# Kernel tuning notes

Measured on AMD Instinct MI355X. Metric: run time of the kernel, lower is better.

The kernel has to match this reference:

```python
import jax, jax.numpy as jnp
import numpy as np

N_NODES = 50000
N_EDGES = 800000
HEADS = 8
CH = 64


def setup_inputs() -> dict:
    key = jax.random.key(0)
    ks = jax.random.split(key, 30)
    rn = lambda k, shape, s=0.1: (jax.random.normal(k, shape, jnp.float32) * s)
    inp = {
        'x': jax.random.normal(ks[0], (N_NODES, 3), jnp.float32),
        'edge_index': jax.random.randint(ks[1], (2, N_EDGES), 0, N_NODES, jnp.int32),
        'edge_attr': jax.random.normal(ks[2], (N_EDGES, 1), jnp.float32),
        'return_attention_weights': 1,
        # node / residual encoders
        'Wn': rn(ks[3], (3, 64)), 'bn': jnp.zeros((64,), jnp.float32),
        'Wr': rn(ks[4], (3, 512)), 'br': jnp.zeros((512,), jnp.float32),
        'W1': rn(ks[5], (64, 512)), 'as1': rn(ks[6], (HEADS, CH)), 'ad1': rn(ks[7], (HEADS, CH)), 'bc1': jnp.zeros((512,), jnp.float32),
        'W2': rn(ks[8], (512, 512)), 'as2': rn(ks[9], (HEADS, CH)), 'ad2': rn(ks[10], (HEADS, CH)), 'bc2': jnp.zeros((512,), jnp.float32),
        'W3': rn(ks[11], (512, 512)), 'as3': rn(ks[12], (HEADS, CH)), 'ad3': rn(ks[13], (HEADS, CH)), 'bc3': jnp.zeros((64,), jnp.float32),
        # node head
        'Wo': rn(ks[14], (64, 2)), 'bo': jnp.zeros((2,), jnp.float32),
        # edge classifier MLP 136 -> 256 -> 2
        'Wm1': rn(ks[15], (136, 256)), 'bm1': jnp.zeros((256,), jnp.float32),
        'Wm2': rn(ks[16], (256, 2)), 'bm2': jnp.zeros((2,), jnp.float32),
    }
    return inp


def _gat(h, src, dst, W, a_src, a_dst, b, concat):
    """PyG GATConv (shared lin, edge_dim=None, eval-mode dropout)."""
    n = h.shape[0]
    g = (h @ W).reshape(n, HEADS, CH)                      # [N,H,C]
    asrc = jnp.sum(g * a_src[None], -1)                    # [N,H]
    adst = jnp.sum(g * a_dst[None], -1)                    # [N,H]
    e = jax.nn.leaky_relu(asrc[src] + adst[dst], 0.2)      # [E',H]
    m = jax.ops.segment_max(e, dst, num_segments=n)        # softmax per destination
    ex = jnp.exp(e - m[dst])
    s = jax.ops.segment_sum(ex, dst, num_segments=n)
    alpha = ex / s[dst]                                    # [E',H]
    out = jax.ops.segment_sum(g[src] * alpha[..., None], dst, num_segments=n)  # [N,H,C]
    out = out.reshape(n, HEADS * CH) if concat else out.mean(axis=1)
    return out + b, alpha


def reference(x, edge_index, edge_attr, return_attention_weights,
              Wn, bn, Wr, br,
              W1, as1, ad1, bc1,
              W2, as2, ad2, bc2,
              W3, as3, ad3, bc3,
              Wo, bo, Wm1, bm1, Wm2, bm2):
    n = x.shape[0]
    e_len = edge_attr.shape[0]
    src0, dst0 = edge_index[0], edge_index[1]
    # GATConv adds self loops internally
    loop = jnp.arange(n, dtype=edge_index.dtype)
    src = jnp.concatenate([src0, loop])
    dst = jnp.concatenate([dst0, loop])

    h = x @ Wn + bn          # node_encoder (dropout is eval identity)
    res = x @ Wr + br        # self.linear residual
    # edge_encoder output is unused by GATConv (edge_dim=None) -> no-op

    o, _ = _gat(h, src, dst, W1, as1, ad1, bc1, concat=True)
    o = jax.nn.elu(o) + res
    o, _ = _gat(o, src, dst, W2, as2, ad2, bc2, concat=True)
    o = jax.nn.elu(o) + res
    o, alpha = _gat(o, src, dst, W3, as3, ad3, bc3, concat=False)
    node_embedding = jax.nn.elu(o)                          # [N,64]

    x_out = node_embedding @ Wo + bo                        # [N,2]
    edge_embedding = jnp.concatenate(
        [node_embedding[src0], alpha[:e_len], node_embedding[dst0]], axis=-1)  # [E,136]
    edge_out = jax.nn.relu(edge_embedding @ Wm1 + bm1) @ Wm2 + bm2             # [E,2]
    return x_out, edge_out
```

## Files before the change

kernel.cpp:

```cpp
#include <hip/hip_runtime.h>
#include <hip/hip_bf16.h>
#include <math.h>

#define N_NODES 50000
#define NPAD    50048
#define N_EDGES 800000
#define EPRIME  (N_EDGES + N_NODES)
#define HEADS 8
#define CH 64
#define FDIM 512

typedef unsigned short ushort_t;
typedef __attribute__((ext_vector_type(8))) short bf16x8_t;
typedef __attribute__((ext_vector_type(4))) float f32x4_t;

__device__ __forceinline__ float bf2f(unsigned short u) {
  union { unsigned int i; float f; } v; v.i = ((unsigned int)u) << 16; return v.f;
}
__device__ __forceinline__ unsigned short f2bf(float f) {
  union { float f; unsigned int i; } v; v.f = f;
  unsigned int x = v.i;
  return (unsigned short)((x + 0x7fffu + ((x >> 16) & 1u)) >> 16);
}
__device__ __forceinline__ float ldf(const void* p, size_t idx, int isf32) {
  return isf32 ? ((const float*)p)[idx] : bf2f(((const ushort_t*)p)[idx]);
}
__device__ __forceinline__ void stf(void* p, size_t idx, float v, int isf32) {
  if (isf32) ((float*)p)[idx] = v;
  else       ((ushort_t*)p)[idx] = f2bf(v);
}
__device__ __forceinline__ float leakyf(float v) { return v >= 0.f ? v : 0.2f * v; }
__device__ __forceinline__ float eluf(float v)   { return v > 0.f ? v : expm1f(v); }

__device__ __forceinline__ float dpp_sum64(float x) {
  x += __int_as_float(__builtin_amdgcn_update_dpp(0, __float_as_int(x), 0xB1, 0xf, 0xf, false));
  x += __int_as_float(__builtin_amdgcn_update_dpp(0, __float_as_int(x), 0x4E, 0xf, 0xf, false));
  x += __int_as_float(__builtin_amdgcn_update_dpp(0, __float_as_int(x), 0x141, 0xf, 0xf, false));
  x += __int_as_float(__builtin_amdgcn_update_dpp(0, __float_as_int(x), 0x140, 0xf, 0xf, false));
  x += __int_as_float(__builtin_amdgcn_update_dpp(0, __float_as_int(x), 0x142, 0xa, 0xf, false));
  x += __int_as_float(__builtin_amdgcn_update_dpp(0, __float_as_int(x), 0x143, 0xc, 0xf, false));
  return x;
}

typedef const __attribute__((address_space(1))) unsigned int* gas1_t;
typedef __attribute__((address_space(3))) unsigned int* las3_t;
__device__ __forceinline__ void gll16(const ushort_t* g, ushort_t* l) {
  __builtin_amdgcn_global_load_lds((gas1_t)g, (las3_t)l, 16, 0, 0);
}

__global__ void detect_dtype(const void* Wn, int* flag) {
  if (blockIdx.x == 0 && threadIdx.x == 0) {
    const ushort_t* u = (const ushort_t*)Wn;
    int extreme = 0;
    for (int i = 0; i < 384; ++i) {
      float v = fabsf(bf2f(u[i]));
      if (v != 0.f && (v > 16.f || v < 6.1e-5f)) extreme++;
    }
    *flag = (extreme >= 20) ? 1 : 0;
  }
}

__global__ void convert_wt(const void* __restrict__ src, ushort_t* __restrict__ dst,
                           int K, int N, int boff, const int* __restrict__ dflag) {
  int isf32 = *dflag;
  int tid = blockIdx.x * blockDim.x + threadIdx.x;
  if (tid >= N * K) return;
  int n = tid / K, k = tid % K;
  dst[tid] = f2bf(ldf(src, (size_t)(boff + k) * N + n, isf32));
}

__global__ void convert_att(const void* s1, const void* d1, const void* s2, const void* d2,
                            const void* s3, const void* d3, ushort_t* __restrict__ dst,
                            const int* __restrict__ dflag) {
  int isf32 = *dflag;
  int tid = blockIdx.x * blockDim.x + threadIdx.x;
  if (tid >= 6 * 512) return;
  int which = tid >> 9, idx = tid & 511;
  const void* p = which == 0 ? s1 : which == 1 ? d1 : which == 2 ? s2
                : which == 3 ? d2 : which == 4 ? s3 : d3;
  dst[tid] = f2bf(ldf(p, idx, isf32));
}

__global__ void init_deg(int* deg, int* fill) {
  int n = blockIdx.x * blockDim.x + threadIdx.x;
  if (n < N_NODES) { deg[n] = 1; fill[n] = 0; }
}

__global__ void count_edges(const int* __restrict__ ei, int* deg) {
  int e = blockIdx.x * blockDim.x + threadIdx.x;
  if (e < N_EDGES) atomicAdd(&deg[ei[N_EDGES + e]], 1);
}

__global__ __launch_bounds__(1024) void scan1024(const int* __restrict__ deg,
                                                 int* __restrict__ rowptr) {
  const int CHUNK = (N_NODES + 1023) / 1024;
  int t = threadIdx.x;
  int wave = t >> 6, lane = t & 63;
  int lo = t * CHUNK;
  int hi = lo + CHUNK; if (hi > N_NODES) hi = N_NODES;
  int s = 0;
  for (int i = lo; i < hi; ++i) s += deg[i];
  int inc = s;
  #pragma unroll
  for (int off = 1; off < 64; off <<= 1) {
    int u = __shfl_up(inc, off);
    if (lane >= off) inc += u;
  }
  __shared__ int wsum[16];
  if (lane == 63) wsum[wave] = inc;
  __syncthreads();
  int wbase = 0;
  for (int w = 0; w < wave; ++w) wbase += wsum[w];
  int run = wbase + inc - s;
  for (int i = lo; i < hi; ++i) { rowptr[i] = run; run += deg[i]; }
  if (t == 1023) rowptr[N_NODES] = run;
}

__global__ void fill_csr(const int* __restrict__ ei, const int* __restrict__ rowptr,
                         int* fill, int* __restrict__ csr_src) {
  int e = blockIdx.x * blockDim.x + threadIdx.x;
  if (e >= EPRIME) return;
  int s, d;
  if (e < N_EDGES) { s = ei[e]; d = ei[N_EDGES + e]; }
  else             { s = d = e - N_EDGES; }
  int pos = rowptr[d] + atomicAdd(&fill[d], 1);
  csr_src[pos] = s;
}

__global__ void encode_h(const void* __restrict__ x, const void* __restrict__ Wn,
                         const void* __restrict__ bn, ushort_t* __restrict__ h,
                         const int* __restrict__ dflag) {
  int isf32 = *dflag;
  int tid = blockIdx.x * blockDim.x + threadIdx.x;
  if (tid >= N_NODES * 64) return;
  int n = tid >> 6, j = tid & 63;
  float x0 = ldf(x, n * 3 + 0, isf32), x1 = ldf(x, n * 3 + 1, isf32), x2 = ldf(x, n * 3 + 2, isf32);
  float v = x0 * ldf(Wn, j, isf32) + x1 * ldf(Wn, 64 + j, isf32)
          + x2 * ldf(Wn, 128 + j, isf32) + ldf(bn, j, isf32);
  h[tid] = f2bf(v);
}

__global__ __launch_bounds__(256) void gemm_bt(
    const ushort_t* __restrict__ A, const ushort_t* __restrict__ BT,
    ushort_t* __restrict__ C, int K, int ldc,
    const ushort_t* __restrict__ att, float* __restrict__ asrc, float* __restrict__ adst)
{
  __shared__ __align__(16) ushort_t As[128][32];
  __shared__ __align__(16) ushort_t Bs[128][32];
  int tid = threadIdx.x;
  int wave = tid >> 6, lane = tid & 63;
  int wr = wave >> 1, wc = wave & 1;
  int row0 = blockIdx.x * 128, col0 = blockIdx.y * 128;
  int fm = lane & 15, fq = lane >> 4;

  f32x4_t acc[4][4];
  #pragma unroll
  for (int i = 0; i < 4; ++i)
    #pragma unroll
    for (int j = 0; j < 4; ++j) acc[i][j] = (f32x4_t){0.f, 0.f, 0.f, 0.f};

  int srow = wave * 32 + (lane >> 2);
  int skel = (lane & 3) * 8;
  const ushort_t* aG0 = A  + (size_t)(row0 + srow) * K + skel;
  const ushort_t* aG1 = A  + (size_t)(row0 + srow + 16) * K + skel;
  const ushort_t* bG0 = BT + (size_t)(col0 + srow) * K + skel;
  const ushort_t* bG1 = BT + (size_t)(col0 + srow + 16) * K + skel;
  ushort_t* aL0 = &As[wave * 32][0];
  ushort_t* aL1 = &As[wave * 32 + 16][0];
  ushort_t* bL0 = &Bs[wave * 32][0];
  ushort_t* bL1 = &Bs[wave * 32 + 16][0];

  for (int k0 = 0; k0 < K; k0 += 32) {
    gll16(aG0 + k0, aL0);
    gll16(aG1 + k0, aL1);
    gll16(bG0 + k0, bL0);
    gll16(bG1 + k0, bL1);
    __syncthreads();
    bf16x8_t af[4], bfr[4];
    #pragma unroll
    for (int i = 0; i < 4; ++i) af[i]  = *(const bf16x8_t*)&As[64 * wr + 16 * i + fm][fq * 8];
    #pragma unroll
    for (int j = 0; j < 4; ++j) bfr[j] = *(const bf16x8_t*)&Bs[64 * wc + 16 * j + fm][fq * 8];
    #pragma unroll
    for (int i = 0; i < 4; ++i)
      #pragma unroll
      for (int j = 0; j < 4; ++j)
        acc[i][j] = __builtin_amdgcn_mfma_f32_16x16x32_bf16(af[i], bfr[j], acc[i][j], 0, 0, 0);
    __syncthreads();
  }

  int do_att = (att != nullptr);
  int head = 2 * blockIdx.y + wc;
  float sa[4], sd[4];
  if (do_att) {
    #pragma unroll
    for (int j = 0; j < 4; ++j) {
      int ch = 16 * j + fm;
      sa[j] = bf2f(att[head * CH + ch]);
      sd[j] = bf2f(att[512 + head * CH + ch]);
    }
  }

  #pragma unroll
  for (int i = 0; i < 4; ++i) {
    int rowb = row0 + 64 * wr + 16 * i + fq * 4;
    #pragma unroll
    for (int r = 0; r < 4; ++r) {
      int row = rowb + r;
      float ss = 0.f, dd = 0.f;
      #pragma unroll
      for (int j = 0; j < 4; ++j) {
        ushort_t uv = f2bf(acc[i][j][r]);
        C[(size_t)row * ldc + col0 + 64 * wc + 16 * j + fm] = uv;
        if (do_att) {
          float cv = bf2f(uv);
          ss += cv * sa[j];
          dd += cv * sd[j];
        }
      }
      if (do_att) {
        #pragma unroll
        for (int off = 8; off > 0; off >>= 1) {
          ss += __shfl_down(ss, off);
          dd += __shfl_down(dd, off);
        }
        if (fm == 0 && row < N_NODES) {
          asrc[row * HEADS + head] = ss;
          adst[row * HEADS + head] = dd;
        }
      }
    }
  }
}

__global__ __launch_bounds__(256) void aggregate(
    const int* __restrict__ rowptr, const int* __restrict__ csr_src,
    const float* __restrict__ asrc, const float* __restrict__ adst,
    float* __restrict__ sumv,
    const ushort_t* __restrict__ g,
    const void* __restrict__ x, const void* __restrict__ Wr,
    const void* __restrict__ br, const void* __restrict__ bc,
    ushort_t* __restrict__ out, int mean_mode,
    const void* __restrict__ Wo, const void* __restrict__ bo,
    void* __restrict__ outh, const int* __restrict__ dflag)
{
  int isf32 = *dflag;
  __shared__ float sx[3];
  int n = blockIdx.x;
  int t = threadIdx.x;
  if (t < 3) sx[t] = ldf(x, n * 3 + t, isf32);
  __syncthreads();

  int start = rowptr[n], end = rowptr[n + 1];
  int c0 = t * 2;
  int h  = t >> 5;
  int i0 = n * HEADS + h;
  float ad = adst[i0];

  float l = 0.f, a0 = 0.f, a1 = 0.f;
  int i = start;
  for (; i + 8 <= end; i += 8) {
    int s[8];
    #pragma unroll
    for (int k = 0; k < 8; ++k) s[k] = csr_src[i + k];
    float e[8];
    unsigned int gv[8];
    #pragma unroll
    for (int k = 0; k < 8; ++k) {
      e[k]  = asrc[s[k] * HEADS + h] + ad;
      gv[k] = *(const unsigned int*)(g + (size_t)s[k] * FDIM + c0);
    }
    #pragma unroll
    for (int k = 0; k < 8; ++k) {
      float p = __expf(leakyf(e[k]));
      l  += p;
      a0 += p * bf2f((ushort_t)(gv[k] & 0xffffu));
      a1 += p * bf2f((ushort_t)(gv[k] >> 16));
    }
  }
  for (; i + 2 <= end; i += 2) {
    int s0 = csr_src[i], s1 = csr_src[i + 1];
    float e0 = asrc[s0 * HEADS + h] + ad;
    float e1 = asrc[s1 * HEADS + h] + ad;
    unsigned int g0 = *(const unsigned int*)(g + (size_t)s0 * FDIM + c0);
    unsigned int g1 = *(const unsigned int*)(g + (size_t)s1 * FDIM + c0);
    float p0 = __expf(leakyf(e0)), p1 = __expf(leakyf(e1));
    l  += p0 + p1;
    a0 += p0 * bf2f((ushort_t)(g0 & 0xffffu)) + p1 * bf2f((ushort_t)(g1 & 0xffffu));
    a1 += p0 * bf2f((ushort_t)(g0 >> 16))     + p1 * bf2f((ushort_t)(g1 >> 16));
  }
  if (i < end) {
    int s0 = csr_src[i];
    float p0 = __expf(leakyf(asrc[s0 * HEADS + h] + ad));
    unsigned int g0 = *(const unsigned int*)(g + (size_t)s0 * FDIM + c0);
    l  += p0;
    a0 += p0 * bf2f((ushort_t)(g0 & 0xffffu));
    a1 += p0 * bf2f((ushort_t)(g0 >> 16));
  }
  a0 /= l;
  a1 /= l;
  if ((t & 31) == 0) sumv[i0] = 1.f / l;

  if (!mean_mode) {
    float r0 = sx[0] * ldf(Wr, c0, isf32)         + sx[1] * ldf(Wr, 512 + c0, isf32)
             + sx[2] * ldf(Wr, 1024 + c0, isf32)  + ldf(br, c0, isf32);
    float r1 = sx[0] * ldf(Wr, c0 + 1, isf32)     + sx[1] * ldf(Wr, 512 + c0 + 1, isf32)
             + sx[2] * ldf(Wr, 1024 + c0 + 1, isf32) + ldf(br, c0 + 1, isf32);
    unsigned int o0 = f2bf(eluf(a0 + ldf(bc, c0, isf32)) + r0);
    unsigned int o1 = f2bf(eluf(a1 + ldf(bc, c0 + 1, isf32)) + r1);
    *(unsigned int*)(out + (size_t)n * FDIM + c0) = o0 | (o1 << 16);
  } else {
    __shared__ float red[512];
    red[c0] = a0; red[c0 + 1] = a1;
    __syncthreads();
    if (t < 64) {
      float tot = 0.f;
      #pragma unroll
      for (int hh = 0; hh < 8; ++hh) tot += red[t + 64 * hh];
      ushort_t uv = f2bf(eluf(tot * 0.125f + ldf(bc, t, isf32)));
      out[(size_t)n * CH + t] = uv;
      float nv = bf2f(uv);
      float p0 = nv * ldf(Wo, t * 2 + 0, isf32);
      float p1 = nv * ldf(Wo, t * 2 + 1, isf32);
      float vv = (t & 1) ? p1 : p0;
      float ww = (t & 1) ? p0 : p1;
      vv += __shfl_xor(ww, 1);
      #pragma unroll
      for (int off = 2; off < 64; off <<= 1) vv += __shfl_xor(vv, off);
      if (t < 2) stf(outh, (size_t)n * 2 + t, vv + ldf(bo, t, isf32), isf32);
    }
  }
}

#define EPW 32
__global__ __launch_bounds__(256) void edge_head6(
    const int* __restrict__ ei, const float* __restrict__ asrc, const float* __restrict__ adst,
    const float* __restrict__ rsumv,
    const ushort_t* __restrict__ pq, const void* __restrict__ Wm1,
    const void* __restrict__ bm1, const void* __restrict__ Wm2,
    const void* __restrict__ bm2, void* __restrict__ out,
    const int* __restrict__ dflag)
{
  int isf32 = *dflag;
  int lane = threadIdx.x & 63;
  int c0 = lane * 4;
  int h = lane & 7;
  float w1r[8][4], w2a[4], w2b[4], b1r[4];
  #pragma unroll
  for (int hh = 0; hh < 8; ++hh)
    #pragma unroll
    for (int j = 0; j < 4; ++j)
      w1r[hh][j] = ldf(Wm1, (64 + hh) * 256 + c0 + j, isf32);
  #pragma unroll
  for (int j = 0; j < 4; ++j) {
    w2a[j] = ldf(Wm2, (c0 + j) * 2 + 0, isf32);
    w2b[j] = ldf(Wm2, (c0 + j) * 2 + 1, isf32);
    b1r[j] = ldf(bm1, c0 + j, isf32);
  }
  float bo0 = ldf(bm2, 0, isf32), bo1 = ldf(bm2, 1, isf32);

  int wid = blockIdx.x * 4 + (threadIdx.x >> 6);
  int e0 = wid * EPW;
  for (int e = e0; e < e0 + EPW; e += 2) {
    int eu = __builtin_amdgcn_readfirstlane(e);
    int sA = ei[eu],     dA = ei[N_EDGES + eu];
    int sB = ei[eu + 1], dB = ei[N_EDGES + eu + 1];
    float vA = asrc[sA * HEADS + h] + adst[dA * HEADS + h];
    float vB = asrc[sB * HEADS + h] + adst[dB * HEADS + h];
    float rsA = rsumv[dA * HEADS + h], rsB = rsumv[dB * HEADS + h];
    ushort4 pvA = *(const ushort4*)(pq + (size_t)sA * FDIM + c0);
    ushort4 qvA = *(const ushort4*)(pq + (size_t)dA * FDIM + 256 + c0);
    ushort4 pvB = *(const ushort4*)(pq + (size_t)sB * FDIM + c0);
    ushort4 qvB = *(const ushort4*)(pq + (size_t)dB * FDIM + 256 + c0);
    float aA = __expf(leakyf(vA)) * rsA;
    float aB = __expf(leakyf(vB)) * rsB;
    float alA[8], alB[8];
    #pragma unroll
    for (int hh = 0; hh < 8; ++hh) {
      alA[hh] = __int_as_float(__builtin_amdgcn_readlane(__float_as_int(aA), hh));
      alB[hh] = __int_as_float(__builtin_amdgcn_readlane(__float_as_int(aB), hh));
    }

    float accA0 = 0.f, accA1 = 0.f, accB0 = 0.f, accB1 = 0.f;
    float pA[4] = { bf2f(pvA.x), bf2f(pvA.y), bf2f(pvA.z), bf2f(pvA.w) };
    float qA[4] = { bf2f(qvA.x), bf2f(qvA.y), bf2f(qvA.z), bf2f(qvA.w) };
    float pB[4] = { bf2f(pvB.x), bf2f(pvB.y), bf2f(pvB.z), bf2f(pvB.w) };
    float qB[4] = { bf2f(qvB.x), bf2f(qvB.y), bf2f(qvB.z), bf2f(qvB.w) };
    #pragma unroll
    for (int j = 0; j < 4; ++j) {
      float hvA = pA[j] + qA[j] + b1r[j];
      float hvB = pB[j] + qB[j] + b1r[j];
      #pragma unroll
      for (int hh = 0; hh < 8; ++hh) {
        hvA += alA[hh] * w1r[hh][j];
        hvB += alB[hh] * w1r[hh][j];
      }
      hvA = fmaxf(hvA, 0.f);
      hvB = fmaxf(hvB, 0.f);
      accA0 += hvA * w2a[j]; accA1 += hvA * w2b[j];
      accB0 += hvB * w2a[j]; accB1 += hvB * w2b[j];
    }
    accA0 = dpp_sum64(accA0);
    accA1 = dpp_sum64(accA1);
    accB0 = dpp_sum64(accB0);
    accB1 = dpp_sum64(accB1);
    if (lane == 63) {
      stf(out, 100000 + (size_t)e * 2 + 0, accA0 + bo0, isf32);
      stf(out, 100000 + (size_t)e * 2 + 1, accA1 + bo1, isf32);
      stf(out, 100000 + (size_t)e * 2 + 2, accB0 + bo0, isf32);
      stf(out, 100000 + (size_t)e * 2 + 3, accB1 + bo1, isf32);
    }
  }
}

extern "C" void kernel_launch(void* const* d_in, const int* in_sizes, int n_in,
                              void* d_out, int out_size, void* d_ws, size_t ws_size,
                              hipStream_t stream) {
  const void* x   = d_in[0];
  const int*  ei  = (const int*)d_in[1];
  const void* Wn  = d_in[4];
  const void* bn  = d_in[5];
  const void* Wr  = d_in[6];
  const void* br  = d_in[7];
  const void* W1  = d_in[8];
  const void* as1 = d_in[9];
  const void* ad1 = d_in[10];
  const void* bc1 = d_in[11];
  const void* W2  = d_in[12];
  const void* as2 = d_in[13];
  const void* ad2 = d_in[14];
  const void* bc2 = d_in[15];
  const void* W3  = d_in[16];
  const void* as3 = d_in[17];
  const void* ad3 = d_in[18];
  const void* bc3 = d_in[19];
  const void* Wo  = d_in[20];
  const void* bo  = d_in[21];
  const void* Wm1 = d_in[22];
  const void* bm1 = d_in[23];
  const void* Wm2 = d_in[24];
  const void* bm2 = d_in[25];

  char* ws = (char*)d_ws;
  size_t off = 0;
  auto take = [&](size_t bytes) -> char* {
    char* p = ws + off;
    off += (bytes + 255) & ~(size_t)255;
    return p;
  };
  ushort_t* h_bf   = (ushort_t*)take((size_t)NPAD * 64 * 2);
  ushort_t* g_bf   = (ushort_t*)take((size_t)NPAD * FDIM * 2);
  ushort_t* o_bf   = (ushort_t*)take((size_t)NPAD * FDIM * 2);
  float*    asrc   = (float*)take((size_t)N_NODES * HEADS * 4);
  float*    adst   = (float*)take((size_t)N_NODES * HEADS * 4);
  float*    sumv   = (float*)take((size_t)N_NODES * HEADS * 4);
  int*      rowptr = (int*)take((size_t)(N_NODES + 1) * 4);
  int*      csr_src= (int*)take((size_t)EPRIME * 4);
  int*      deg    = (int*)take((size_t)N_NODES * 4);
  int*      fillc  = (int*)take((size_t)N_NODES * 4);
  int*      dflag  = (int*)take(256);
  ushort_t* WT1    = (ushort_t*)take((size_t)512 * 64 * 2);
  ushort_t* WT2    = (ushort_t*)take((size_t)512 * 512 * 2);
  ushort_t* WT3    = (ushort_t*)take((size_t)512 * 512 * 2);
  ushort_t* WTPQ   = (ushort_t*)take((size_t)512 * 64 * 2);
  ushort_t* attv   = (ushort_t*)take((size_t)6 * 512 * 2);

  dim3 b256(256);
  const int MB = NPAD / 128;

  detect_dtype<<<dim3(1), dim3(64), 0, stream>>>(Wn, dflag);

  convert_wt<<<dim3(128),  b256, 0, stream>>>(W1, WT1, 64, 512, 0, dflag);
  convert_wt<<<dim3(1024), b256, 0, stream>>>(W2, WT2, 512, 512, 0, dflag);
  convert_wt<<<dim3(1024), b256, 0, stream>>>(W3, WT3, 512, 512, 0, dflag);
  convert_wt<<<dim3(64),   b256, 0, stream>>>(Wm1, WTPQ,            64, 256, 0,  dflag);
  convert_wt<<<dim3(64),   b256, 0, stream>>>(Wm1, WTPQ + 256 * 64, 64, 256, 72, dflag);
  convert_att<<<dim3(12),  b256, 0, stream>>>(as1, ad1, as2, ad2, as3, ad3, attv, dflag);

  init_deg<<<dim3((N_NODES + 255) / 256), b256, 0, stream>>>(deg, fillc);
  count_edges<<<dim3((N_EDGES + 255) / 256), b256, 0, stream>>>(ei, deg);
  scan1024<<<dim3(1), dim3(1024), 0, stream>>>(deg, rowptr);
  fill_csr<<<dim3((EPRIME + 255) / 256), b256, 0, stream>>>(ei, rowptr, fillc, csr_src);

  encode_h<<<dim3((N_NODES * 64 + 255) / 256), b256, 0, stream>>>(x, Wn, bn, h_bf, dflag);

  gemm_bt<<<dim3(MB, 4), b256, 0, stream>>>(h_bf, WT1, g_bf, 64, 512,
                                            attv, asrc, adst);
  aggregate<<<dim3(N_NODES), b256, 0, stream>>>(rowptr, csr_src, asrc, adst, sumv,
                                                g_bf, x, Wr, br, bc1, o_bf, 0,
                                                nullptr, nullptr, d_out, dflag);

  gemm_bt<<<dim3(MB, 4), b256, 0, stream>>>(o_bf, WT2, g_bf, 512, 512,
                                            attv + 1024, asrc, adst);
  aggregate<<<dim3(N_NODES), b256, 0, stream>>>(rowptr, csr_src, asrc, adst, sumv,
                                                g_bf, x, Wr, br, bc2, o_bf, 0,
                                                nullptr, nullptr, d_out, dflag);

  gemm_bt<<<dim3(MB, 4), b256, 0, stream>>>(o_bf, WT3, g_bf, 512, 512,
                                            attv + 2048, asrc, adst);
  aggregate<<<dim3(N_NODES), b256, 0, stream>>>(rowptr, csr_src, asrc, adst, sumv,
                                                g_bf, x, Wr, br, bc3, h_bf, 1,
                                                Wo, bo, d_out, dflag);

  gemm_bt<<<dim3(MB, 4), b256, 0, stream>>>(h_bf, WTPQ, g_bf, 64, 512,
                                            nullptr, nullptr, nullptr);
  edge_head6<<<dim3(N_EDGES / (EPW * 4)), b256, 0, stream>>>(ei, asrc, adst, sumv, g_bf,
                                                             Wm1, bm1, Wm2, bm2,
                                                             d_out, dflag);
}
```

Before: 1.075 ms.

## Split aggregation edges across waves with 16-byte gathers and LDS reduction

The per-node aggregation kernel now has each of the four waves handle every fourth incoming edge. Each lane gathers eight bf16 channels with one 16-byte load instead of two channels with a 4-byte load. Per-wave partial sums and softmax denominators are combined through shared memory before the bias, ELU and residual epilogue. This aims to raise memory-level parallelism and use wider loads for the irregular row gathers, at the cost of extra LDS traffic, an additional barrier, and more registers per thread.

```diff
diff --git a/kernel.cpp b/kernel.cpp
--- a/kernel.cpp
+++ b/kernel.cpp
@@ -233,7 +233,7 @@
   }
 }
 
-__global__ __launch_bounds__(256) void aggregate(
+__global__ __launch_bounds__(256) void aggregate2(
     const int* __restrict__ rowptr, const int* __restrict__ csr_src,
     const float* __restrict__ asrc, const float* __restrict__ adst,
     float* __restrict__ sumv,
@@ -245,61 +245,65 @@
     void* __restrict__ outh, const int* __restrict__ dflag)
 {
   int isf32 = *dflag;
+  __shared__ float red[4][512];
+  __shared__ float lred[4][8];
   __shared__ float sx[3];
   int n = blockIdx.x;
   int t = threadIdx.x;
+  int wave = t >> 6, lane = t & 63;
   if (t < 3) sx[t] = ldf(x, n * 3 + t, isf32);
+
+  int ch0 = lane * 8;
+  int hh  = lane >> 3;
+  int start = rowptr[n], end = rowptr[n + 1];
+  float ad = adst[n * HEADS + hh];
+
+  float acc[8];
+  #pragma unroll
+  for (int k = 0; k < 8; ++k) acc[k] = 0.f;
+  float l = 0.f;
+
+  int i = start + wave;
+  for (; i + 4 < end; i += 8) {
+    int iu0 = __builtin_amdgcn_readfirstlane(i);
+    int iu1 = __builtin_amdgcn_readfirstlane(i + 4);
+    int s0 = csr_src[iu0];
+    int s1 = csr_src[iu1];
+    float e0 = asrc[s0 * HEADS + hh] + ad;
+    float e1 = asrc[s1 * HEADS + hh] + ad;
+    bf16x8_t gv0 = *(const bf16x8_t*)(g + (size_t)s0 * FDIM + ch0);
+    bf16x8_t gv1 = *(const bf16x8_t*)(g + (size_t)s1 * FDIM + ch0);
+    float p0 = __expf(leakyf(e0));
+    float p1 = __expf(leakyf(e1));
+    l += p0 + p1;
+    #pragma unroll
+    for (int k = 0; k < 8; ++k)
+      acc[k] += p0 * bf2f((ushort_t)gv0[k]) + p1 * bf2f((ushort_t)gv1[k]);
+  }
+  if (i < end) {
+    int iu0 = __builtin_amdgcn_readfirstlane(i);
+    int s0 = csr_src[iu0];
+    float e0 = asrc[s0 * HEADS + hh] + ad;
+    bf16x8_t gv0 = *(const bf16x8_t*)(g + (size_t)s0 * FDIM + ch0);
+    float p0 = __expf(leakyf(e0));
+    l += p0;
+    #pragma unroll
+    for (int k = 0; k < 8; ++k) acc[k] += p0 * bf2f((ushort_t)gv0[k]);
+  }
+
+  #pragma unroll
+  for (int k = 0; k < 8; ++k) red[wave][ch0 + k] = acc[k];
+  if ((lane & 7) == 0) lred[wave][hh] = l;
   __syncthreads();
 
-  int start = rowptr[n], end = rowptr[n + 1];
   int c0 = t * 2;
   int h  = t >> 5;
-  int i0 = n * HEADS + h;
-  float ad = adst[i0];
-
-  float l = 0.f, a0 = 0.f, a1 = 0.f;
-  int i = start;
-  for (; i + 8 <= end; i += 8) {
-    int s[8];
-    #pragma unroll
-    for (int k = 0; k < 8; ++k) s[k] = csr_src[i + k];
-    float e[8];
-    unsigned int gv[8];
-    #pragma unroll
-    for (int k = 0; k < 8; ++k) {
-      e[k]  = asrc[s[k] * HEADS + h] + ad;
-      gv[k] = *(const unsigned int*)(g + (size_t)s[k] * FDIM + c0);
-    }
-    #pragma unroll
-    for (int k = 0; k < 8; ++k) {
-      float p = __expf(leakyf(e[k]));
-      l  += p;
-      a0 += p * bf2f((ushort_t)(gv[k] & 0xffffu));
-      a1 += p * bf2f((ushort_t)(gv[k] >> 16));
-    }
-  }
-  for (; i + 2 <= end; i += 2) {
-    int s0 = csr_src[i], s1 = csr_src[i + 1];
-    float e0 = asrc[s0 * HEADS + h] + ad;
-    float e1 = asrc[s1 * HEADS + h] + ad;
-    unsigned int g0 = *(const unsigned int*)(g + (size_t)s0 * FDIM + c0);
-    unsigned int g1 = *(const unsigned int*)(g + (size_t)s1 * FDIM + c0);
-    float p0 = __expf(leakyf(e0)), p1 = __expf(leakyf(e1));
-    l  += p0 + p1;
-    a0 += p0 * bf2f((ushort_t)(g0 & 0xffffu)) + p1 * bf2f((ushort_t)(g1 & 0xffffu));
-    a1 += p0 * bf2f((ushort_t)(g0 >> 16))     + p1 * bf2f((ushort_t)(g1 >> 16));
-  }
-  if (i < end) {
-    int s0 = csr_src[i];
-    float p0 = __expf(leakyf(asrc[s0 * HEADS + h] + ad));
-    unsigned int g0 = *(const unsigned int*)(g + (size_t)s0 * FDIM + c0);
-    l  += p0;
-    a0 += p0 * bf2f((ushort_t)(g0 & 0xffffu));
-    a1 += p0 * bf2f((ushort_t)(g0 >> 16));
-  }
-  a0 /= l;
-  a1 /= l;
-  if ((t & 31) == 0) sumv[i0] = 1.f / l;
+  float a0 = red[0][c0]     + red[1][c0]     + red[2][c0]     + red[3][c0];
+  float a1 = red[0][c0 + 1] + red[1][c0 + 1] + red[2][c0 + 1] + red[3][c0 + 1];
+  float lt = lred[0][h] + lred[1][h] + lred[2][h] + lred[3][h];
+  a0 /= lt;
+  a1 /= lt;
+  if ((t & 31) == 0) sumv[n * HEADS + h] = 1.f / lt;
 
   if (!mean_mode) {
     float r0 = sx[0] * ldf(Wr, c0, isf32)         + sx[1] * ldf(Wr, 512 + c0, isf32)
@@ -310,13 +314,13 @@
     unsigned int o1 = f2bf(eluf(a1 + ldf(bc, c0 + 1, isf32)) + r1);
     *(unsigned int*)(out + (size_t)n * FDIM + c0) = o0 | (o1 << 16);
   } else {
-    __shared__ float red[512];
-    red[c0] = a0; red[c0 + 1] = a1;
+    __syncthreads();
+    red[0][c0] = a0; red[0][c0 + 1] = a1;
     __syncthreads();
     if (t < 64) {
       float tot = 0.f;
       #pragma unroll
-      for (int hh = 0; hh < 8; ++hh) tot += red[t + 64 * hh];
+      for (int hh2 = 0; hh2 < 8; ++hh2) tot += red[0][t + 64 * hh2];
       ushort_t uv = f2bf(eluf(tot * 0.125f + ldf(bc, t, isf32)));
       out[(size_t)n * CH + t] = uv;
       float nv = bf2f(uv);
@@ -486,21 +490,21 @@
 
   gemm_bt<<<dim3(MB, 4), b256, 0, stream>>>(h_bf, WT1, g_bf, 64, 512,
                                             attv, asrc, adst);
-  aggregate<<<dim3(N_NODES), b256, 0, stream>>>(rowptr, csr_src, asrc, adst, sumv,
-                                                g_bf, x, Wr, br, bc1, o_bf, 0,
-                                                nullptr, nullptr, d_out, dflag);
+  aggregate2<<<dim3(N_NODES), b256, 0, stream>>>(rowptr, csr_src, asrc, adst, sumv,
+                                                 g_bf, x, Wr, br, bc1, o_bf, 0,
+                                                 nullptr, nullptr, d_out, dflag);
 
   gemm_bt<<<dim3(MB, 4), b256, 0, stream>>>(o_bf, WT2, g_bf, 512, 512,
                                             attv + 1024, asrc, adst);
-  aggregate<<<dim3(N_NODES), b256, 0, stream>>>(rowptr, csr_src, asrc, adst, sumv,
-                                                g_bf, x, Wr, br, bc2, o_bf, 0,
-                                                nullptr, nullptr, d_out, dflag);
+  aggregate2<<<dim3(N_NODES), b256, 0, stream>>>(rowptr, csr_src, asrc, adst, sumv,
+                                                 g_bf, x, Wr, br, bc2, o_bf, 0,
+                                                 nullptr, nullptr, d_out, dflag);
 
   gemm_bt<<<dim3(MB, 4), b256, 0, stream>>>(o_bf, WT3, g_bf, 512, 512,
                                             attv + 2048, asrc, adst);
-  aggregate<<<dim3(N_NODES), b256, 0, stream>>>(rowptr, csr_src, asrc, adst, sumv,
-                                                g_bf, x, Wr, br, bc3, h_bf, 1,
-                                                Wo, bo, d_out, dflag);
+  aggregate2<<<dim3(N_NODES), b256, 0, stream>>>(rowptr, csr_src, asrc, adst, sumv,
+                                                 g_bf, x, Wr, br, bc3, h_bf, 1,
+                                                 Wo, bo, d_out, dflag);
 
   gemm_bt<<<dim3(MB, 4), b256, 0, stream>>>(h_bf, WTPQ, g_bf, 64, 512,
                                             nullptr, nullptr, nullptr);
```

Measured after the change: 1.030 ms. -4.2%, faster.
